# Optimization experiments

Hardware: AMD Instinct MI355X
Metric: run time of the kernel (lower is better)

The kernel has to match this reference:

```python
import jax, jax.numpy as jnp
import numpy as np
from jax import lax

PATCH = 15
WIDTH_DCP = 55


def _box_sum(x, r):
    # AvgPool2d(kernel=2r+1, stride=1, padding=r, count_include_pad=True) * (2r+1)^2;
    # the kernel-size factor cancels in all mean_*/N ratios below.
    return lax.reduce_window(x, 0.0, lax.add, (1, 1, 2 * r + 1, 2 * r + 1),
                             (1, 1, 1, 1), ((0, 0), (0, 0), (r, r), (r, r)))


def _guided_filter(I, p, r, eps):
    Nn = _box_sum(jnp.ones_like(p), r)
    mean_I = _box_sum(I, r) / Nn
    mean_p = _box_sum(p, r) / Nn
    mean_Ip = _box_sum(I * p, r) / Nn
    cov_Ip = mean_Ip - mean_I * mean_p
    mean_II = _box_sum(I * I, r) / Nn
    var_I = mean_II - mean_I * mean_I
    a = cov_Ip / (var_I + eps)
    b = mean_p - a * mean_I
    mean_a = _box_sum(a, r) / Nn
    mean_b = _box_sum(b, r) / Nn
    return mean_a * I + mean_b


def _dark_channel(x):
    d = x.min(axis=1, keepdims=True)
    pad = WIDTH_DCP // 2
    d = jnp.pad(d, ((0, 0), (0, 0), (pad, pad), (pad, pad)), constant_values=1.0)
    return lax.reduce_window(d, jnp.inf, lax.min, (1, 1, WIDTH_DCP, WIDTH_DCP),
                             (1, 1, 1, 1), 'VALID')


def _map_A(x):
    N, C, H, W = x.shape
    dc = _dark_channel(x).reshape(N, -1)
    k = int(H * W * 0.001)
    _, idx = lax.top_k(dc, k)  # brightest dark-channel pixels
    xr = x.reshape(N, 3, -1)
    searched = jnp.take_along_axis(xr, jnp.broadcast_to(idx[:, None, :], (N, 3, k)), axis=2)
    A = searched.mean(axis=2)
    return jnp.broadcast_to(A[:, :, None, None], x.shape)


def _t_bccr(haze, mapA, ps):
    t1 = (mapA - haze) / (mapA - 20.0 / 255.0)
    t2 = (mapA - haze) / (mapA - 300.0 / 255.0)
    t = jnp.maximum(t1, t2).max(axis=1, keepdims=True)
    pad = ps // 2
    t = jnp.pad(t, ((0, 0), (0, 0), (pad, pad), (pad, pad)), constant_values=0.0)
    t = lax.reduce_window(t, -jnp.inf, lax.max, (1, 1, ps, ps), (1, 1, 1, 1), 'VALID')
    return jnp.clip(t, 0.05, 1.0)


def _pad_reshape(data, ps):
    N, C, H, W = data.shape
    pad_H = (ps - H % ps) % ps
    pad_W = (ps - W % ps) % ps
    padded = jnp.pad(data, ((0, 0), (0, 0), (pad_H // 2, pad_H - pad_H // 2),
                            (pad_W // 2, pad_W - pad_W // 2)), mode='edge')
    nH = padded.shape[2] // ps
    nW = padded.shape[3] // ps
    p = padded[:, 0].reshape(N, nH, ps, nW, ps).transpose(0, 1, 3, 2, 4)
    p = p.reshape(N, nH * nW, ps * ps).transpose(0, 2, 1)  # [N, ps*ps, P]
    return p, pad_H // 2, pad_W // 2, nH, nW


def _transmission(S, V1, ps, pixel_number=10, slp_length=0.1):
    X, sH, sW, nH, nW = _pad_reshape(V1, ps)  # [N, pp, P]
    Y, _, _, _, _ = _pad_reshape(S, ps)
    dX = X[:, :, None, :] - X[:, None, :, :]          # [N, pp, pp, P]
    dY = Y[:, :, None, :] - Y[:, None, :, :]
    slope = dY / (dX + 1e-8)
    smask = ((slope > -1) & (slope < 0)).astype(X.dtype)
    scount = smask.sum(axis=2)                         # [N, pp, P]
    pmask = (scount >= 0.5 * ps * ps).astype(X.dtype)
    pcount = pmask.sum(axis=1, keepdims=True)          # [N, 1, P]
    mx = (X * pmask).sum(axis=1, keepdims=True) / (pcount + 1e-5)
    my = (Y * pmask).sum(axis=1, keepdims=True) / (pcount + 1e-5)
    k = ((X * Y * pmask).sum(axis=1, keepdims=True) - pcount * mx * my) / (
        ((X * pmask) ** 2).sum(axis=1, keepdims=True) - pcount * mx ** 2 + 1e-5)
    b = my - k * mx
    t = 1.0 + k / (b + 1e-8)
    length = (1.0 + k ** 2) ** 0.5 * ((X * pmask).max(axis=1, keepdims=True)
                                      - (X + 1e8 * (1.0 - pmask)).min(axis=1, keepdims=True))
    tmask = ((pcount > pixel_number) & (length > slp_length) & (k > -1) & (k < 0)
             & (t > 0.01) & (t < 1 - 0.01)).astype(X.dtype)
    t = (t * tmask).reshape(-1, 1, nH, nW)
    t = jnp.repeat(jnp.repeat(t, ps, axis=2), ps, axis=3)  # nearest upsample x ps
    return t[:, :, sH:S.shape[2] + sH, sW:S.shape[3] + sW]


def _percentile(t, bili=0.05):
    N = t.shape[0]
    flat = jnp.where(t > 0, t, 10.0).reshape(N, -1)
    s = jnp.sort(flat, axis=1)
    n = flat.shape[1]
    idx = min(int(bili * n), n - 1)
    return s[:, idx].reshape(-1, 1, 1, 1)


def _restore(image, ps=PATCH):
    mapA = _map_A(image)
    norm = image / mapA
    mx = norm.max(axis=1, keepdims=True)
    S = 1.0 - norm.min(axis=1, keepdims=True) / (mx + 1e-8)
    V1 = 1.0 / (mx + 1e-8)
    t1 = _transmission(S, V1, ps)
    half = ps // 2
    t2 = _transmission(S[:, :, half:, half:], V1[:, :, half:, half:], ps)
    t2 = jnp.pad(t2, ((0, 0), (0, 0), (half, 0), (half, 0)), constant_values=0.0)
    t_slp = jnp.where((t1 != 0) & (t2 != 0), (t1 + t2) / 2.0,
                      jnp.where(t1 != 0, t1, t2))
    t_bl = _t_bccr(image, mapA, ps)
    t_min = _percentile(t_slp)
    t_fusion = jnp.clip(jnp.where(t_slp > 0, t_slp, t_bl), t_min, 1.0)
    t_ref = _guided_filter(image.mean(axis=1, keepdims=True), t_fusion, 2 * ps, 1e-3)
    return (image - mapA) / t_ref + mapA


def setup_inputs() -> dict:
    key = jax.random.key(0)
    image = jax.random.uniform(key, (1, 3, 480, 480), dtype=jnp.float32)
    return {"image": image}


def reference(image):
    return _restore(image)
```

## Files before the change

kernel.cpp:

```cpp
#include <hip/hip_runtime.h>
#include <math.h>

#define W 480
#define HT 480
#define HW (W*HT)
#define GE (HW/256)
#define PP 225
#define NPATCH 1024
#define EQCAP 8192

struct State {
  unsigned slotP[4];
  unsigned slotK[4];
  float sumA[3];
  unsigned eqCount;
  float A[3];
  unsigned tminbits;
  unsigned eqIdx[EQCAP];
  float tp1[NPATCH];
  float tp2[NPATCH];
};

__device__ __forceinline__ void resolve_level(const unsigned* __restrict__ h,
                                              unsigned k_in, int desc,
                                              unsigned* lds,
                                              unsigned& chosen, unsigned& k_out) {
  int t = threadIdx.x;
  unsigned c = h[desc ? (255 - t) : t];
  lds[t] = c;
  __syncthreads();
  for (int s = 1; s < 256; s <<= 1) {
    unsigned add = (t >= s) ? lds[t - s] : 0u;
    __syncthreads();
    lds[t] += add;
    __syncthreads();
  }
  unsigned incl = lds[t];
  unsigned excl = incl - c;
  if (incl >= k_in && excl < k_in) { lds[256] = (unsigned)t; lds[257] = k_in - excl; }
  __syncthreads();
  unsigned tt = lds[256];
  k_out = lds[257];
  chosen = desc ? (255u - tt) : tt;
  __syncthreads();
}

__global__ __launch_bounds__(512) void k_rowmin(const float* __restrict__ img,
                                                float* __restrict__ rowmin,
                                                State* st, unsigned* __restrict__ hist16) {
  __shared__ float l[534];
  int y = blockIdx.x, t = threadIdx.x;
  int g = y * 512 + t;
  if (g < 65536) hist16[g] = 0u;
  for (int i = t; i < 534; i += 512) {
    int col = i - 27;
    float v = 1.0f;
    if ((unsigned)col < (unsigned)W) {
      int q = y * W + col;
      v = fminf(fminf(img[q], img[HW + q]), img[2 * HW + q]);
    }
    l[i] = v;
  }
  if (g == 0) { st->sumA[0] = 0.f; st->sumA[1] = 0.f; st->sumA[2] = 0.f; st->eqCount = 0u; }
  __syncthreads();
  if (t < W) {
    float m = l[t];
    for (int d = 1; d < 55; ++d) m = fminf(m, l[t + d]);
    rowmin[y * W + t] = m;
  }
}

__global__ __launch_bounds__(256) void k_minV3(const float* __restrict__ rowmin,
                                               float* __restrict__ dc,
                                               unsigned* __restrict__ hist16) {
  __shared__ unsigned short bs[256];
  int t = threadIdx.x;
  int p = blockIdx.x * 256 + t;
  int y = p / W, x = p - y * W;
  int lo = y - 27, hi = y + 27;
  float m = (lo < 0 || hi >= HT) ? 1.0f : INFINITY;
  int lo2 = max(lo, 0), hi2 = min(hi, HT - 1);
  for (int yy = lo2; yy <= hi2; ++yy) m = fminf(m, rowmin[yy * W + x]);
  dc[p] = m;
  unsigned b16 = __float_as_uint(m) >> 16;
  bs[t] = (unsigned short)b16;
  __syncthreads();
  int firstIdx = 256, cnt = 0;
  for (int j = 0; j < 256; ++j) {
    if ((unsigned)bs[j] == b16) { ++cnt; if (j < firstIdx) firstIdx = j; }
  }
  if (firstIdx == t) atomicAdd(&hist16[b16], (unsigned)cnt);
}

__global__ __launch_bounds__(256) void k_resolve16(const unsigned* __restrict__ hist16,
                                                   State* st) {
  __shared__ unsigned lds[258];
  __shared__ unsigned lh[256];
  int t = threadIdx.x;
  const uint4* h4 = (const uint4*)hist16;
  unsigned s = 0;
  for (int i = 0; i < 64; ++i) { uint4 v = h4[t * 64 + i]; s += v.x + v.y + v.z + v.w; }
  lh[t] = s;
  __syncthreads();
  unsigned ct, kc;
  resolve_level(lh, 230u, 1, lds, ct, kc);
  lh[t] = hist16[ct * 256 + t];
  __syncthreads();
  unsigned b, kp;
  resolve_level(lh, kc, 1, lds, b, kp);
  if (t == 0) { st->slotP[0] = (ct << 8) | b; st->slotK[0] = kp; }
}

__global__ __launch_bounds__(256) void k_gather2(const float* __restrict__ dc,
                                                 const float* __restrict__ img, State* st) {
  __shared__ float ls[3];
  __shared__ unsigned lcnt, lbase;
  int t = threadIdx.x;
  if (t == 0) { ls[0] = 0.f; ls[1] = 0.f; ls[2] = 0.f; lcnt = 0u; }
  __syncthreads();
  int p = blockIdx.x * 256 + t;
  unsigned p16 = st->slotP[0];
  unsigned b16 = __float_as_uint(dc[p]) >> 16;
  bool eq = (b16 == p16);
  unsigned my = 0;
  if (b16 > p16) {
    atomicAdd(&ls[0], img[p]);
    atomicAdd(&ls[1], img[HW + p]);
    atomicAdd(&ls[2], img[2 * HW + p]);
  } else if (eq) {
    my = atomicAdd(&lcnt, 1u);
  }
  __syncthreads();
  if (t == 0 && lcnt) lbase = atomicAdd(&st->eqCount, lcnt);
  __syncthreads();
  if (eq) { unsigned pos = lbase + my; if (pos < (unsigned)EQCAP) st->eqIdx[pos] = (unsigned)p; }
  if (t == 0 && (ls[0] != 0.f || ls[1] != 0.f || ls[2] != 0.f)) {
    atomicAdd(&st->sumA[0], ls[0]);
    atomicAdd(&st->sumA[1], ls[1]);
    atomicAdd(&st->sumA[2], ls[2]);
  }
}

__global__ __launch_bounds__(256) void k_finalizeA2(const float* __restrict__ dc,
                                                    const float* __restrict__ img, State* st) {
  __shared__ unsigned lds[258];
  __shared__ unsigned lh[256];
  __shared__ unsigned sIdx[EQCAP];
  __shared__ unsigned short sVal[EQCAP];
  __shared__ float ssum[3];
  int t = threadIdx.x;
  unsigned k = st->slotK[0];
  unsigned ne = st->eqCount; if (ne > (unsigned)EQCAP) ne = EQCAP;
  for (int i = t; i < (int)ne; i += 256) {
    unsigned q = st->eqIdx[i];
    sIdx[i] = q;
    sVal[i] = (unsigned short)(__float_as_uint(dc[q]) & 0xFFFFu);
  }
  if (t < 3) ssum[t] = 0.f;
  __syncthreads();
  unsigned vpfx = 0u;
  for (int lev = 0; lev < 2; ++lev) {
    int s = 8 - 8 * lev;
    lh[t] = 0u;
    __syncthreads();
    for (int i = t; i < (int)ne; i += 256) {
      unsigned v = (unsigned)sVal[i];
      if (lev == 0 || (v >> 8) == (vpfx >> 8))
        atomicAdd(&lh[(v >> s) & 0xFFu], 1u);
    }
    __syncthreads();
    unsigned ch, kn;
    resolve_level(lh, k, 1, lds, ch, kn);
    vpfx |= ch << s;
    k = kn;
  }
  unsigned pfx = 0u;
  for (int lev = 0; lev < 3; ++lev) {
    int s = 16 - 8 * lev;
    lh[t] = 0u;
    __syncthreads();
    for (int i = t; i < (int)ne; i += 256) {
      if ((unsigned)sVal[i] == vpfx) {
        unsigned v = sIdx[i];
        if ((v >> (s + 8)) == (pfx >> (s + 8)))
          atomicAdd(&lh[(v >> s) & 0xFFu], 1u);
      }
    }
    __syncthreads();
    unsigned ch, kn;
    resolve_level(lh, k, 0, lds, ch, kn);
    pfx |= ch << s;
    k = kn;
  }
  float a0 = 0.f, a1 = 0.f, a2 = 0.f;
  for (int i = t; i < (int)ne; i += 256) {
    unsigned v = (unsigned)sVal[i], q = sIdx[i];
    if (v > vpfx || (v == vpfx && q <= pfx)) {
      a0 += img[q]; a1 += img[HW + q]; a2 += img[2 * HW + q];
    }
  }
  atomicAdd(&ssum[0], a0); atomicAdd(&ssum[1], a1); atomicAdd(&ssum[2], a2);
  __syncthreads();
  if (t == 0) {
    st->A[0] = (st->sumA[0] + ssum[0]) / 230.0f;
    st->A[1] = (st->sumA[1] + ssum[1]) / 230.0f;
    st->A[2] = (st->sumA[2] + ssum[2]) / 230.0f;
  }
}

__device__ __forceinline__ float wred_sum(float v) { for (int m = 32; m; m >>= 1) v += __shfl_xor(v, m, 64); return v; }
__device__ __forceinline__ float wred_max(float v) { for (int m = 32; m; m >>= 1) v = fmaxf(v, __shfl_xor(v, m, 64)); return v; }
__device__ __forceinline__ float wred_min(float v) { for (int m = 32; m; m >>= 1) v = fminf(v, __shfl_xor(v, m, 64)); return v; }

__global__ __launch_bounds__(256) void k_mega1(const float* __restrict__ img,
                                               float* __restrict__ mh, State* st) {
  __shared__ float2 XY[PP];
  __shared__ float part[4][8];
  __shared__ float Tl[494];
  int b = blockIdx.x;
  int t = threadIdx.x;
  float A0 = st->A[0], A1 = st->A[1], A2 = st->A[2];
  const float c20 = (float)(20.0 / 255.0);
  const float c300 = (float)(300.0 / 255.0);
  if (b >= 2048) {
    int y = b - 2048;
    for (int i = t; i < 494; i += 256) {
      int col = i - 7;
      float v = 0.0f;
      if ((unsigned)col < (unsigned)W) {
        int q = y * W + col;
        float r = img[q], g = img[HW + q], bl = img[2 * HW + q];
        float t0 = fmaxf((A0 - r) / (A0 - c20), (A0 - r) / (A0 - c300));
        float t1 = fmaxf((A1 - g) / (A1 - c20), (A1 - g) / (A1 - c300));
        float t2 = fmaxf((A2 - bl) / (A2 - c20), (A2 - bl) / (A2 - c300));
        v = fmaxf(fmaxf(t0, t1), t2);
      }
      Tl[i] = v;
    }
    __syncthreads();
    for (int x = t; x < W; x += 256) {
      float m = -INFINITY;
      for (int d = 0; d < 15; ++d) m = fmaxf(m, Tl[x + d]);
      mh[y * W + x] = m;
    }
    return;
  }
  int mode = b >> 10;
  int pid = b & 1023;
  int ph = pid >> 5, pw = pid & 31;
  if (t < PP) {
    int r = t / 15, c = t - (t / 15) * 15;
    int y, x;
    if (mode == 0) { y = ph * 15 + r; x = pw * 15 + c; }
    else {
      y = ph * 15 + r + 4; y = (y < 7) ? 7 : ((y > 479) ? 479 : y);
      x = pw * 15 + c + 4; x = (x < 7) ? 7 : ((x > 479) ? 479 : x);
    }
    int q = y * W + x;
    float rr = img[q], gg = img[HW + q], bb = img[2 * HW + q];
    float nr = rr / A0, ng = gg / A1, nb = bb / A2;
    float mx = fmaxf(fmaxf(nr, ng), nb);
    float mn = fminf(fminf(nr, ng), nb);
    float d = mx + 1e-8f;
    XY[t] = make_float2(1.0f / d, 1.0f - mn / d);
  }
  __syncthreads();
  float xi = 0.f, yi = 0.f;
  int cnt = 0;
  if (t < PP) {
    xi = XY[t].x; yi = XY[t].y;
    #pragma unroll 5
    for (int j = 0; j < PP; ++j) {
      float2 o = XY[j];
      float dY = yi - o.y;
      float D = (xi - o.x) + 1e-8f;
      cnt += ((dY * D < 0.0f) && (fabsf(dY) < fabsf(D))) ? 1 : 0;
    }
  }
  float pmf = (t < PP && cnt >= 113) ? 1.0f : 0.0f;
  float xm = xi * pmf, ym = yi * pmf;
  float v0 = wred_sum(pmf);
  float v1 = wred_sum(xm);
  float v2 = wred_sum(ym);
  float v3 = wred_sum(xm * ym);
  float v4 = wred_sum(xm * xm);
  float v5 = wred_max((t < PP) ? xm : -INFINITY);
  float v6 = wred_min((t < PP) ? (xi + 1e8f * (1.0f - pmf)) : INFINITY);
  int wid = t >> 6, lane = t & 63;
  if (lane == 0) {
    part[wid][0] = v0; part[wid][1] = v1; part[wid][2] = v2; part[wid][3] = v3;
    part[wid][4] = v4; part[wid][5] = v5; part[wid][6] = v6;
  }
  __syncthreads();
  if (t == 0) {
    float pcount = 0.f, sx = 0.f, sy = 0.f, sxy = 0.f, sxx = 0.f;
    float mxX = -INFINITY, mnX = INFINITY;
    for (int w2 = 0; w2 < 4; ++w2) {
      pcount += part[w2][0]; sx += part[w2][1]; sy += part[w2][2];
      sxy += part[w2][3]; sxx += part[w2][4];
      mxX = fmaxf(mxX, part[w2][5]); mnX = fminf(mnX, part[w2][6]);
    }
    float den = pcount + 1e-5f;
    float mxv = sx / den, myv = sy / den;
    float kk = (sxy - pcount * mxv * myv) / (sxx - pcount * (mxv * mxv) + 1e-5f);
    float bb = myv - kk * mxv;
    float tt = 1.0f + kk / (bb + 1e-8f);
    float len = sqrtf(1.0f + kk * kk) * (mxX - mnX);
    bool m = (pcount > 10.0f) && (len > 0.1f) && (kk > -1.0f) && (kk < 0.0f)
             && (tt > 0.01f) && (tt < 0.99f);
    float res = tt * (m ? 1.0f : 0.0f);
    if (mode == 0) st->tp1[pid] = res; else st->tp2[pid] = res;
  }
}

__global__ __launch_bounds__(256) void k_maxV_pct(const float* __restrict__ mh,
                                                  float* __restrict__ tb, State* st) {
  __shared__ unsigned lh[256];
  __shared__ unsigned lds[258];
  __shared__ float tp1s[NPATCH], tp2s[NPATCH];
  int b = blockIdx.x;
  int t = threadIdx.x;
  if (b < GE) {
    int p = b * 256 + t;
    int y = p / W, x = p - y * W;
    float m = -INFINITY;
    for (int d = -7; d <= 7; ++d) {
      int yy = y + d;
      float v = ((unsigned)yy < (unsigned)HT) ? mh[yy * W + x] : 0.0f;
      m = fmaxf(m, v);
    }
    tb[p] = fminf(fmaxf(m, 0.05f), 1.0f);
    return;
  }
  for (int i = t; i < NPATCH; i += 256) { tp1s[i] = st->tp1[i]; tp2s[i] = st->tp2[i]; }
  __syncthreads();
  unsigned prefix = 0u, k = 11521u;
  for (int level = 0; level < 4; ++level) {
    lh[t] = 0u;
    __syncthreads();
    unsigned mask = (level == 0) ? 0u : (0xFFFFFFFFu << (32 - 8 * level));
    int shift = 24 - 8 * level;
    for (int i = t; i < NPATCH; i += 256) {
      int ph = i >> 5, pw = i & 31;
      float a = tp1s[i];
      int rcnt[2], ridx[2], ccnt[2], cidx[2];
      if (ph == 0) { rcnt[0] = 7; ridx[0] = -1; rcnt[1] = 8; ridx[1] = 0; }
      else         { rcnt[0] = 4; ridx[0] = ph - 1; rcnt[1] = 11; ridx[1] = ph; }
      if (pw == 0) { ccnt[0] = 7; cidx[0] = -1; ccnt[1] = 8; cidx[1] = 0; }
      else         { ccnt[0] = 4; cidx[0] = pw - 1; ccnt[1] = 11; cidx[1] = pw; }
      for (int ri = 0; ri < 2; ++ri)
        for (int ci = 0; ci < 2; ++ci) {
          unsigned area = (unsigned)(rcnt[ri] * ccnt[ci]);
          float bb = 0.0f;
          if (ridx[ri] >= 0 && cidx[ci] >= 0) bb = tp2s[ridx[ri] * 32 + cidx[ci]];
          float r;
          if (a != 0.0f && bb != 0.0f) r = (a + bb) / 2.0f;
          else r = (a != 0.0f) ? a : bb;
          float u = (r > 0.0f) ? r : 10.0f;
          unsigned bits = __float_as_uint(u);
          if ((bits & mask) == prefix)
            atomicAdd(&lh[(bits >> shift) & 0xFFu], area);
        }
    }
    __syncthreads();
    unsigned ch, kn;
    resolve_level(lh, k, 0, lds, ch, kn);
    prefix |= ch << shift;
    k = kn;
  }
  if (t == 0) st->tminbits = prefix;
}

__global__ __launch_bounds__(512) void k_gf1h(const float* __restrict__ img,
                                              const float* __restrict__ tb,
                                              const State* __restrict__ st,
                                              float4* __restrict__ box4) {
  __shared__ float tp1s[NPATCH], tp2s[NPATCH];
  __shared__ float Pl[540], Il[540];
  int y = blockIdx.x, t = threadIdx.x;
  for (int i = t; i < NPATCH; i += 512) { tp1s[i] = st->tp1[i]; tp2s[i] = st->tp2[i]; }
  __syncthreads();
  float tmin = __uint_as_float(st->tminbits);
  int c1row = (y / 15) * 32;
  bool c2ok = (y >= 7);
  int c2row = c2ok ? ((y - 4) / 15) * 32 : 0;
  for (int i = t; i < 540; i += 512) {
    int col = i - 30;
    float pv = 0.0f, iv = 0.0f;
    if ((unsigned)col < (unsigned)W) {
      int q = y * W + col;
      float a = tp1s[c1row + col / 15];
      float bb = 0.0f;
      if (c2ok && col >= 7) bb = tp2s[c2row + (col - 4) / 15];
      float r;
      if (a != 0.0f && bb != 0.0f) r = (a + bb) / 2.0f;
      else r = (a != 0.0f) ? a : bb;
      float v = (r > 0.0f) ? r : tb[q];
      v = (v < tmin) ? tmin : v;
      v = (v > 1.0f) ? 1.0f : v;
      pv = v;
      iv = ((img[q] + img[HW + q]) + img[2 * HW + q]) / 3.0f;
    }
    Pl[i] = pv; Il[i] = iv;
  }
  __syncthreads();
  if (t < W) {
    float sI = 0.f, sP = 0.f, sIp = 0.f, sII = 0.f;
    for (int d = 0; d < 61; ++d) {
      float iv = Il[t + d], pv = Pl[t + d];
      sI += iv; sP += pv; sIp += iv * pv; sII += iv * iv;
    }
    box4[y * W + t] = make_float4(sI, sP, sIp, sII);
  }
}

__global__ __launch_bounds__(512) void k_gf1vh(const float4* __restrict__ box4,
                                               float2* __restrict__ hab) {
  __shared__ float2 l[540];
  int y = blockIdx.x, t = threadIdx.x;
  float2 v = make_float2(0.f, 0.f);
  if (t < W) {
    float sI = 0.f, sP = 0.f, sIp = 0.f, sII = 0.f;
    for (int d = -30; d <= 30; ++d) {
      int yy = y + d;
      if ((unsigned)yy < (unsigned)HT) {
        float4 b = box4[yy * W + t];
        sI += b.x; sP += b.y; sIp += b.z; sII += b.w;
      }
    }
    int ny = min(y + 30, HT - 1) - max(y - 30, 0) + 1;
    int nx = min(t + 30, W - 1) - max(t - 30, 0) + 1;
    float Nn = (float)(ny * nx);
    float mI = sI / Nn, mP = sP / Nn, mIp = sIp / Nn, mII = sII / Nn;
    float cov = mIp - mI * mP;
    float var = mII - mI * mI;
    float av = cov / (var + 1e-3f);
    v = make_float2(av, mP - av * mI);
  }
  if (t < 30) { l[t] = make_float2(0.f, 0.f); l[510 + t] = make_float2(0.f, 0.f); }
  if (t < W) l[30 + t] = v;
  __syncthreads();
  if (t < W) {
    float sa = 0.f, sb = 0.f;
    for (int d = 0; d < 61; ++d) { float2 u = l[t + d]; sa += u.x; sb += u.y; }
    hab[y * W + t] = make_float2(sa, sb);
  }
}

__global__ __launch_bounds__(256) void k_gf2vfin(const float2* __restrict__ hab,
                                                 const float* __restrict__ img,
                                                 const State* __restrict__ st,
                                                 float* __restrict__ out) {
  int p = blockIdx.x * 256 + threadIdx.x;
  int y = p / W, x = p - y * W;
  float sa = 0.f, sb = 0.f;
  for (int d = -30; d <= 30; ++d) {
    int yy = y + d;
    if ((unsigned)yy < (unsigned)HT) { float2 v = hab[yy * W + x]; sa += v.x; sb += v.y; }
  }
  int ny = min(y + 30, HT - 1) - max(y - 30, 0) + 1;
  int nx = min(x + 30, W - 1) - max(x - 30, 0) + 1;
  float Nn = (float)(ny * nx);
  float r = img[p], g = img[HW + p], bl = img[2 * HW + p];
  float Iv = ((r + g) + bl) / 3.0f;
  float tref = (sa / Nn) * Iv + (sb / Nn);
  float A0 = st->A[0], A1 = st->A[1], A2 = st->A[2];
  out[p]          = (r  - A0) / tref + A0;
  out[HW + p]     = (g  - A1) / tref + A1;
  out[2 * HW + p] = (bl - A2) / tref + A2;
}

extern "C" void kernel_launch(void* const* d_in, const int* in_sizes, int n_in,
                              void* d_out, int out_size, void* d_ws, size_t ws_size,
                              hipStream_t stream) {
  (void)in_sizes; (void)n_in; (void)out_size; (void)ws_size;
  const float* img = (const float*)d_in[0];
  float* out = (float*)d_out;
  State* st = (State*)d_ws;
  unsigned* hist16 = (unsigned*)((char*)d_ws + 65536);
  float* sb = (float*)((char*)d_ws + 65536 + 262144);
  float* bufA = sb;
  float* bufB = sb + HW;
  float4* box4 = (float4*)(sb + 2 * HW);
  float2* hab  = (float2*)(sb + 6 * HW);

  dim3 b256(256), b512(512);
  dim3 ge(GE), rows(HT);

  k_rowmin<<<rows, b512, 0, stream>>>(img, bufB, st, hist16);
  k_minV3<<<ge, b256, 0, stream>>>(bufB, bufA, hist16);
  k_resolve16<<<dim3(1), b256, 0, stream>>>(hist16, st);
  k_gather2<<<ge, b256, 0, stream>>>(bufA, img, st);
  k_finalizeA2<<<dim3(1), b256, 0, stream>>>(bufA, img, st);
  k_mega1<<<dim3(2048 + HT), b256, 0, stream>>>(img, bufB, st);
  k_maxV_pct<<<dim3(GE + 1), b256, 0, stream>>>(bufB, bufA, st);
  k_gf1h<<<rows, b512, 0, stream>>>(img, bufA, st, box4);
  k_gf1vh<<<rows, b512, 0, stream>>>(box4, hab);
  k_gf2vfin<<<ge, b256, 0, stream>>>(hab, img, st, out);
}
```

Before: 185.5 us.

## Fuse all pipeline stages into one cooperative persistent kernel with grid syncs

Replaces the ten separate kernel launches with a single cooperative kernel of 512 persistent blocks that loops over rows and tiles for each stage and separates stages with grid-wide syncs. Serial single-block stages run on block 0 while the other blocks wait at the next grid sync. This targets per-launch overhead and inter-kernel gaps. The cost is that 512-thread row kernels now run as 256-thread blocks striding over rows, so parallelism per stage is capped at the grid size, and each grid sync adds its own latency.

```diff
diff --git a/kernel.cpp b/kernel.cpp
--- a/kernel.cpp
+++ b/kernel.cpp
@@ -1,13 +1,17 @@
 #include <hip/hip_runtime.h>
+#include <hip/hip_cooperative_groups.h>
 #include <math.h>
 
 #define W 480
 #define HT 480
 #define HW (W*HT)
-#define GE (HW/256)
+#define NT (HW/256)
 #define PP 225
 #define NPATCH 1024
 #define EQCAP 8192
+#define GRID 512
+
+namespace cg = cooperative_groups;
 
 struct State {
   unsigned slotP[4];
@@ -45,429 +49,442 @@
   __syncthreads();
 }
 
-__global__ __launch_bounds__(512) void k_rowmin(const float* __restrict__ img,
-                                                float* __restrict__ rowmin,
-                                                State* st, unsigned* __restrict__ hist16) {
-  __shared__ float l[534];
-  int y = blockIdx.x, t = threadIdx.x;
-  int g = y * 512 + t;
-  if (g < 65536) hist16[g] = 0u;
-  for (int i = t; i < 534; i += 512) {
-    int col = i - 27;
-    float v = 1.0f;
-    if ((unsigned)col < (unsigned)W) {
-      int q = y * W + col;
-      v = fminf(fminf(img[q], img[HW + q]), img[2 * HW + q]);
-    }
-    l[i] = v;
-  }
-  if (g == 0) { st->sumA[0] = 0.f; st->sumA[1] = 0.f; st->sumA[2] = 0.f; st->eqCount = 0u; }
-  __syncthreads();
-  if (t < W) {
-    float m = l[t];
-    for (int d = 1; d < 55; ++d) m = fminf(m, l[t + d]);
-    rowmin[y * W + t] = m;
-  }
-}
-
-__global__ __launch_bounds__(256) void k_minV3(const float* __restrict__ rowmin,
-                                               float* __restrict__ dc,
-                                               unsigned* __restrict__ hist16) {
-  __shared__ unsigned short bs[256];
-  int t = threadIdx.x;
-  int p = blockIdx.x * 256 + t;
-  int y = p / W, x = p - y * W;
-  int lo = y - 27, hi = y + 27;
-  float m = (lo < 0 || hi >= HT) ? 1.0f : INFINITY;
-  int lo2 = max(lo, 0), hi2 = min(hi, HT - 1);
-  for (int yy = lo2; yy <= hi2; ++yy) m = fminf(m, rowmin[yy * W + x]);
-  dc[p] = m;
-  unsigned b16 = __float_as_uint(m) >> 16;
-  bs[t] = (unsigned short)b16;
-  __syncthreads();
-  int firstIdx = 256, cnt = 0;
-  for (int j = 0; j < 256; ++j) {
-    if ((unsigned)bs[j] == b16) { ++cnt; if (j < firstIdx) firstIdx = j; }
-  }
-  if (firstIdx == t) atomicAdd(&hist16[b16], (unsigned)cnt);
-}
-
-__global__ __launch_bounds__(256) void k_resolve16(const unsigned* __restrict__ hist16,
-                                                   State* st) {
-  __shared__ unsigned lds[258];
-  __shared__ unsigned lh[256];
-  int t = threadIdx.x;
-  const uint4* h4 = (const uint4*)hist16;
-  unsigned s = 0;
-  for (int i = 0; i < 64; ++i) { uint4 v = h4[t * 64 + i]; s += v.x + v.y + v.z + v.w; }
-  lh[t] = s;
-  __syncthreads();
-  unsigned ct, kc;
-  resolve_level(lh, 230u, 1, lds, ct, kc);
-  lh[t] = hist16[ct * 256 + t];
-  __syncthreads();
-  unsigned b, kp;
-  resolve_level(lh, kc, 1, lds, b, kp);
-  if (t == 0) { st->slotP[0] = (ct << 8) | b; st->slotK[0] = kp; }
-}
-
-__global__ __launch_bounds__(256) void k_gather2(const float* __restrict__ dc,
-                                                 const float* __restrict__ img, State* st) {
-  __shared__ float ls[3];
-  __shared__ unsigned lcnt, lbase;
-  int t = threadIdx.x;
-  if (t == 0) { ls[0] = 0.f; ls[1] = 0.f; ls[2] = 0.f; lcnt = 0u; }
-  __syncthreads();
-  int p = blockIdx.x * 256 + t;
-  unsigned p16 = st->slotP[0];
-  unsigned b16 = __float_as_uint(dc[p]) >> 16;
-  bool eq = (b16 == p16);
-  unsigned my = 0;
-  if (b16 > p16) {
-    atomicAdd(&ls[0], img[p]);
-    atomicAdd(&ls[1], img[HW + p]);
-    atomicAdd(&ls[2], img[2 * HW + p]);
-  } else if (eq) {
-    my = atomicAdd(&lcnt, 1u);
-  }
-  __syncthreads();
-  if (t == 0 && lcnt) lbase = atomicAdd(&st->eqCount, lcnt);
-  __syncthreads();
-  if (eq) { unsigned pos = lbase + my; if (pos < (unsigned)EQCAP) st->eqIdx[pos] = (unsigned)p; }
-  if (t == 0 && (ls[0] != 0.f || ls[1] != 0.f || ls[2] != 0.f)) {
-    atomicAdd(&st->sumA[0], ls[0]);
-    atomicAdd(&st->sumA[1], ls[1]);
-    atomicAdd(&st->sumA[2], ls[2]);
-  }
-}
-
-__global__ __launch_bounds__(256) void k_finalizeA2(const float* __restrict__ dc,
-                                                    const float* __restrict__ img, State* st) {
-  __shared__ unsigned lds[258];
-  __shared__ unsigned lh[256];
-  __shared__ unsigned sIdx[EQCAP];
-  __shared__ unsigned short sVal[EQCAP];
-  __shared__ float ssum[3];
-  int t = threadIdx.x;
-  unsigned k = st->slotK[0];
-  unsigned ne = st->eqCount; if (ne > (unsigned)EQCAP) ne = EQCAP;
-  for (int i = t; i < (int)ne; i += 256) {
-    unsigned q = st->eqIdx[i];
-    sIdx[i] = q;
-    sVal[i] = (unsigned short)(__float_as_uint(dc[q]) & 0xFFFFu);
-  }
-  if (t < 3) ssum[t] = 0.f;
-  __syncthreads();
-  unsigned vpfx = 0u;
-  for (int lev = 0; lev < 2; ++lev) {
-    int s = 8 - 8 * lev;
-    lh[t] = 0u;
-    __syncthreads();
-    for (int i = t; i < (int)ne; i += 256) {
-      unsigned v = (unsigned)sVal[i];
-      if (lev == 0 || (v >> 8) == (vpfx >> 8))
-        atomicAdd(&lh[(v >> s) & 0xFFu], 1u);
-    }
-    __syncthreads();
-    unsigned ch, kn;
-    resolve_level(lh, k, 1, lds, ch, kn);
-    vpfx |= ch << s;
-    k = kn;
-  }
-  unsigned pfx = 0u;
-  for (int lev = 0; lev < 3; ++lev) {
-    int s = 16 - 8 * lev;
-    lh[t] = 0u;
-    __syncthreads();
-    for (int i = t; i < (int)ne; i += 256) {
-      if ((unsigned)sVal[i] == vpfx) {
-        unsigned v = sIdx[i];
-        if ((v >> (s + 8)) == (pfx >> (s + 8)))
-          atomicAdd(&lh[(v >> s) & 0xFFu], 1u);
-      }
-    }
-    __syncthreads();
-    unsigned ch, kn;
-    resolve_level(lh, k, 0, lds, ch, kn);
-    pfx |= ch << s;
-    k = kn;
-  }
-  float a0 = 0.f, a1 = 0.f, a2 = 0.f;
-  for (int i = t; i < (int)ne; i += 256) {
-    unsigned v = (unsigned)sVal[i], q = sIdx[i];
-    if (v > vpfx || (v == vpfx && q <= pfx)) {
-      a0 += img[q]; a1 += img[HW + q]; a2 += img[2 * HW + q];
-    }
-  }
-  atomicAdd(&ssum[0], a0); atomicAdd(&ssum[1], a1); atomicAdd(&ssum[2], a2);
-  __syncthreads();
-  if (t == 0) {
-    st->A[0] = (st->sumA[0] + ssum[0]) / 230.0f;
-    st->A[1] = (st->sumA[1] + ssum[1]) / 230.0f;
-    st->A[2] = (st->sumA[2] + ssum[2]) / 230.0f;
-  }
-}
-
 __device__ __forceinline__ float wred_sum(float v) { for (int m = 32; m; m >>= 1) v += __shfl_xor(v, m, 64); return v; }
 __device__ __forceinline__ float wred_max(float v) { for (int m = 32; m; m >>= 1) v = fmaxf(v, __shfl_xor(v, m, 64)); return v; }
 __device__ __forceinline__ float wred_min(float v) { for (int m = 32; m; m >>= 1) v = fminf(v, __shfl_xor(v, m, 64)); return v; }
 
-__global__ __launch_bounds__(256) void k_mega1(const float* __restrict__ img,
-                                               float* __restrict__ mh, State* st) {
-  __shared__ float2 XY[PP];
-  __shared__ float part[4][8];
-  __shared__ float Tl[494];
-  int b = blockIdx.x;
-  int t = threadIdx.x;
-  float A0 = st->A[0], A1 = st->A[1], A2 = st->A[2];
-  const float c20 = (float)(20.0 / 255.0);
-  const float c300 = (float)(300.0 / 255.0);
-  if (b >= 2048) {
-    int y = b - 2048;
-    for (int i = t; i < 494; i += 256) {
-      int col = i - 7;
-      float v = 0.0f;
-      if ((unsigned)col < (unsigned)W) {
-        int q = y * W + col;
-        float r = img[q], g = img[HW + q], bl = img[2 * HW + q];
-        float t0 = fmaxf((A0 - r) / (A0 - c20), (A0 - r) / (A0 - c300));
-        float t1 = fmaxf((A1 - g) / (A1 - c20), (A1 - g) / (A1 - c300));
-        float t2 = fmaxf((A2 - bl) / (A2 - c20), (A2 - bl) / (A2 - c300));
-        v = fmaxf(fmaxf(t0, t1), t2);
-      }
-      Tl[i] = v;
-    }
+__global__ __launch_bounds__(256, 2) void k_all(const float* __restrict__ img,
+                                                float* __restrict__ out,
+                                                State* __restrict__ st,
+                                                unsigned* __restrict__ hist16,
+                                                float* __restrict__ bufA,
+                                                float* __restrict__ bufB,
+                                                float4* __restrict__ box4,
+                                                float2* __restrict__ hab) {
+  __shared__ __align__(16) char smem[51264];
+  unsigned* s_lds = (unsigned*)smem;
+  unsigned* s_lh  = (unsigned*)(smem + 1040);
+  char* ph = smem + 2080;
+  cg::grid_group grid = cg::this_grid();
+  const int t = threadIdx.x;
+  const int bid = blockIdx.x;
+  const int nb = gridDim.x;
+
+  {
+    int g = bid * 256 + t;
+    if (g < 65536) hist16[g] = 0u;
+    if (g == 0) { st->sumA[0] = 0.f; st->sumA[1] = 0.f; st->sumA[2] = 0.f; st->eqCount = 0u; }
+  }
+  {
+    float* l = (float*)ph;
+    for (int y = bid; y < HT; y += nb) {
+      for (int i = t; i < 534; i += 256) {
+        int col = i - 27;
+        float v = 1.0f;
+        if ((unsigned)col < (unsigned)W) {
+          int q = y * W + col;
+          v = fminf(fminf(img[q], img[HW + q]), img[2 * HW + q]);
+        }
+        l[i] = v;
+      }
+      __syncthreads();
+      for (int x = t; x < W; x += 256) {
+        float m = l[x];
+        for (int d = 1; d < 55; ++d) m = fminf(m, l[x + d]);
+        bufB[y * W + x] = m;
+      }
+      __syncthreads();
+    }
+  }
+  grid.sync();
+  {
+    unsigned short* bs = (unsigned short*)ph;
+    for (int vb = bid; vb < NT; vb += nb) {
+      int p = vb * 256 + t;
+      int y = p / W, x = p - y * W;
+      int lo = y - 27, hi = y + 27;
+      float m = (lo < 0 || hi >= HT) ? 1.0f : INFINITY;
+      int lo2 = max(lo, 0), hi2 = min(hi, HT - 1);
+      for (int yy = lo2; yy <= hi2; ++yy) m = fminf(m, bufB[yy * W + x]);
+      bufA[p] = m;
+      unsigned b16 = __float_as_uint(m) >> 16;
+      bs[t] = (unsigned short)b16;
+      __syncthreads();
+      int firstIdx = 256, cnt = 0;
+      for (int j = 0; j < 256; ++j) {
+        if ((unsigned)bs[j] == b16) { ++cnt; if (j < firstIdx) firstIdx = j; }
+      }
+      if (firstIdx == t) atomicAdd(&hist16[b16], (unsigned)cnt);
+      __syncthreads();
+    }
+  }
+  grid.sync();
+  if (bid == 0) {
+    const uint4* h4 = (const uint4*)hist16;
+    unsigned s = 0;
+    for (int i = 0; i < 64; ++i) { uint4 v = h4[t * 64 + i]; s += v.x + v.y + v.z + v.w; }
+    s_lh[t] = s;
     __syncthreads();
-    for (int x = t; x < W; x += 256) {
-      float m = -INFINITY;
-      for (int d = 0; d < 15; ++d) m = fmaxf(m, Tl[x + d]);
-      mh[y * W + x] = m;
-    }
-    return;
-  }
-  int mode = b >> 10;
-  int pid = b & 1023;
-  int ph = pid >> 5, pw = pid & 31;
-  if (t < PP) {
-    int r = t / 15, c = t - (t / 15) * 15;
-    int y, x;
-    if (mode == 0) { y = ph * 15 + r; x = pw * 15 + c; }
-    else {
-      y = ph * 15 + r + 4; y = (y < 7) ? 7 : ((y > 479) ? 479 : y);
-      x = pw * 15 + c + 4; x = (x < 7) ? 7 : ((x > 479) ? 479 : x);
-    }
-    int q = y * W + x;
-    float rr = img[q], gg = img[HW + q], bb = img[2 * HW + q];
-    float nr = rr / A0, ng = gg / A1, nb = bb / A2;
-    float mx = fmaxf(fmaxf(nr, ng), nb);
-    float mn = fminf(fminf(nr, ng), nb);
-    float d = mx + 1e-8f;
-    XY[t] = make_float2(1.0f / d, 1.0f - mn / d);
-  }
-  __syncthreads();
-  float xi = 0.f, yi = 0.f;
-  int cnt = 0;
-  if (t < PP) {
-    xi = XY[t].x; yi = XY[t].y;
-    #pragma unroll 5
-    for (int j = 0; j < PP; ++j) {
-      float2 o = XY[j];
-      float dY = yi - o.y;
-      float D = (xi - o.x) + 1e-8f;
-      cnt += ((dY * D < 0.0f) && (fabsf(dY) < fabsf(D))) ? 1 : 0;
-    }
-  }
-  float pmf = (t < PP && cnt >= 113) ? 1.0f : 0.0f;
-  float xm = xi * pmf, ym = yi * pmf;
-  float v0 = wred_sum(pmf);
-  float v1 = wred_sum(xm);
-  float v2 = wred_sum(ym);
-  float v3 = wred_sum(xm * ym);
-  float v4 = wred_sum(xm * xm);
-  float v5 = wred_max((t < PP) ? xm : -INFINITY);
-  float v6 = wred_min((t < PP) ? (xi + 1e8f * (1.0f - pmf)) : INFINITY);
-  int wid = t >> 6, lane = t & 63;
-  if (lane == 0) {
-    part[wid][0] = v0; part[wid][1] = v1; part[wid][2] = v2; part[wid][3] = v3;
-    part[wid][4] = v4; part[wid][5] = v5; part[wid][6] = v6;
-  }
-  __syncthreads();
-  if (t == 0) {
-    float pcount = 0.f, sx = 0.f, sy = 0.f, sxy = 0.f, sxx = 0.f;
-    float mxX = -INFINITY, mnX = INFINITY;
-    for (int w2 = 0; w2 < 4; ++w2) {
-      pcount += part[w2][0]; sx += part[w2][1]; sy += part[w2][2];
-      sxy += part[w2][3]; sxx += part[w2][4];
-      mxX = fmaxf(mxX, part[w2][5]); mnX = fminf(mnX, part[w2][6]);
-    }
-    float den = pcount + 1e-5f;
-    float mxv = sx / den, myv = sy / den;
-    float kk = (sxy - pcount * mxv * myv) / (sxx - pcount * (mxv * mxv) + 1e-5f);
-    float bb = myv - kk * mxv;
-    float tt = 1.0f + kk / (bb + 1e-8f);
-    float len = sqrtf(1.0f + kk * kk) * (mxX - mnX);
-    bool m = (pcount > 10.0f) && (len > 0.1f) && (kk > -1.0f) && (kk < 0.0f)
-             && (tt > 0.01f) && (tt < 0.99f);
-    float res = tt * (m ? 1.0f : 0.0f);
-    if (mode == 0) st->tp1[pid] = res; else st->tp2[pid] = res;
-  }
-}
-
-__global__ __launch_bounds__(256) void k_maxV_pct(const float* __restrict__ mh,
-                                                  float* __restrict__ tb, State* st) {
-  __shared__ unsigned lh[256];
-  __shared__ unsigned lds[258];
-  __shared__ float tp1s[NPATCH], tp2s[NPATCH];
-  int b = blockIdx.x;
-  int t = threadIdx.x;
-  if (b < GE) {
-    int p = b * 256 + t;
-    int y = p / W, x = p - y * W;
-    float m = -INFINITY;
-    for (int d = -7; d <= 7; ++d) {
-      int yy = y + d;
-      float v = ((unsigned)yy < (unsigned)HT) ? mh[yy * W + x] : 0.0f;
-      m = fmaxf(m, v);
-    }
-    tb[p] = fminf(fmaxf(m, 0.05f), 1.0f);
-    return;
-  }
-  for (int i = t; i < NPATCH; i += 256) { tp1s[i] = st->tp1[i]; tp2s[i] = st->tp2[i]; }
-  __syncthreads();
-  unsigned prefix = 0u, k = 11521u;
-  for (int level = 0; level < 4; ++level) {
-    lh[t] = 0u;
+    unsigned ct, kc;
+    resolve_level(s_lh, 230u, 1, s_lds, ct, kc);
+    s_lh[t] = hist16[ct * 256 + t];
     __syncthreads();
-    unsigned mask = (level == 0) ? 0u : (0xFFFFFFFFu << (32 - 8 * level));
-    int shift = 24 - 8 * level;
-    for (int i = t; i < NPATCH; i += 256) {
-      int ph = i >> 5, pw = i & 31;
-      float a = tp1s[i];
-      int rcnt[2], ridx[2], ccnt[2], cidx[2];
-      if (ph == 0) { rcnt[0] = 7; ridx[0] = -1; rcnt[1] = 8; ridx[1] = 0; }
-      else         { rcnt[0] = 4; ridx[0] = ph - 1; rcnt[1] = 11; ridx[1] = ph; }
-      if (pw == 0) { ccnt[0] = 7; cidx[0] = -1; ccnt[1] = 8; cidx[1] = 0; }
-      else         { ccnt[0] = 4; cidx[0] = pw - 1; ccnt[1] = 11; cidx[1] = pw; }
-      for (int ri = 0; ri < 2; ++ri)
-        for (int ci = 0; ci < 2; ++ci) {
-          unsigned area = (unsigned)(rcnt[ri] * ccnt[ci]);
+    unsigned b, kp;
+    resolve_level(s_lh, kc, 1, s_lds, b, kp);
+    if (t == 0) { st->slotP[0] = (ct << 8) | b; st->slotK[0] = kp; }
+  }
+  grid.sync();
+  {
+    float* ls = (float*)ph;
+    unsigned* lu = (unsigned*)(ph + 16);
+    unsigned p16 = st->slotP[0];
+    for (int vb = bid; vb < NT; vb += nb) {
+      if (t == 0) { ls[0] = 0.f; ls[1] = 0.f; ls[2] = 0.f; lu[0] = 0u; }
+      __syncthreads();
+      int p = vb * 256 + t;
+      unsigned b16 = __float_as_uint(bufA[p]) >> 16;
+      bool eq = (b16 == p16);
+      unsigned my = 0;
+      if (b16 > p16) {
+        atomicAdd(&ls[0], img[p]);
+        atomicAdd(&ls[1], img[HW + p]);
+        atomicAdd(&ls[2], img[2 * HW + p]);
+      } else if (eq) {
+        my = atomicAdd(&lu[0], 1u);
+      }
+      __syncthreads();
+      if (t == 0 && lu[0]) lu[1] = atomicAdd(&st->eqCount, lu[0]);
+      __syncthreads();
+      if (eq) { unsigned pos = lu[1] + my; if (pos < (unsigned)EQCAP) st->eqIdx[pos] = (unsigned)p; }
+      if (t == 0 && (ls[0] != 0.f || ls[1] != 0.f || ls[2] != 0.f)) {
+        atomicAdd(&st->sumA[0], ls[0]);
+        atomicAdd(&st->sumA[1], ls[1]);
+        atomicAdd(&st->sumA[2], ls[2]);
+      }
+      __syncthreads();
+    }
+  }
+  grid.sync();
+  if (bid == 0) {
+    float* ssum = (float*)ph;
+    unsigned short* sVal = (unsigned short*)(ph + 16);
+    unsigned* sIdx = (unsigned*)(ph + 16 + 2 * EQCAP);
+    unsigned k = st->slotK[0];
+    unsigned ne = st->eqCount; if (ne > (unsigned)EQCAP) ne = EQCAP;
+    for (int i = t; i < (int)ne; i += 256) {
+      unsigned q = st->eqIdx[i];
+      sIdx[i] = q;
+      sVal[i] = (unsigned short)(__float_as_uint(bufA[q]) & 0xFFFFu);
+    }
+    if (t < 3) ssum[t] = 0.f;
+    __syncthreads();
+    unsigned vpfx = 0u;
+    for (int lev = 0; lev < 2; ++lev) {
+      int s = 8 - 8 * lev;
+      s_lh[t] = 0u;
+      __syncthreads();
+      for (int i = t; i < (int)ne; i += 256) {
+        unsigned v = (unsigned)sVal[i];
+        if (lev == 0 || (v >> 8) == (vpfx >> 8))
+          atomicAdd(&s_lh[(v >> s) & 0xFFu], 1u);
+      }
+      __syncthreads();
+      unsigned ch, kn;
+      resolve_level(s_lh, k, 1, s_lds, ch, kn);
+      vpfx |= ch << s;
+      k = kn;
+    }
+    unsigned pfx = 0u;
+    for (int lev = 0; lev < 3; ++lev) {
+      int s = 16 - 8 * lev;
+      s_lh[t] = 0u;
+      __syncthreads();
+      for (int i = t; i < (int)ne; i += 256) {
+        if ((unsigned)sVal[i] == vpfx) {
+          unsigned v = sIdx[i];
+          if ((v >> (s + 8)) == (pfx >> (s + 8)))
+            atomicAdd(&s_lh[(v >> s) & 0xFFu], 1u);
+        }
+      }
+      __syncthreads();
+      unsigned ch, kn;
+      resolve_level(s_lh, k, 0, s_lds, ch, kn);
+      pfx |= ch << s;
+      k = kn;
+    }
+    float a0 = 0.f, a1 = 0.f, a2 = 0.f;
+    for (int i = t; i < (int)ne; i += 256) {
+      unsigned v = (unsigned)sVal[i], q = sIdx[i];
+      if (v > vpfx || (v == vpfx && q <= pfx)) {
+        a0 += img[q]; a1 += img[HW + q]; a2 += img[2 * HW + q];
+      }
+    }
+    atomicAdd(&ssum[0], a0); atomicAdd(&ssum[1], a1); atomicAdd(&ssum[2], a2);
+    __syncthreads();
+    if (t == 0) {
+      st->A[0] = (st->sumA[0] + ssum[0]) / 230.0f;
+      st->A[1] = (st->sumA[1] + ssum[1]) / 230.0f;
+      st->A[2] = (st->sumA[2] + ssum[2]) / 230.0f;
+    }
+  }
+  grid.sync();
+  {
+    float A0 = st->A[0], A1 = st->A[1], A2 = st->A[2];
+    const float c20 = (float)(20.0 / 255.0);
+    const float c300 = (float)(300.0 / 255.0);
+    float2* XY = (float2*)ph;
+    float* part = (float*)(ph + 1808);
+    float* Tl = (float*)(ph + 1952);
+    for (int vb = bid; vb < 2048 + HT; vb += nb) {
+      if (vb >= 2048) {
+        int y = vb - 2048;
+        for (int i = t; i < 494; i += 256) {
+          int col = i - 7;
+          float v = 0.0f;
+          if ((unsigned)col < (unsigned)W) {
+            int q = y * W + col;
+            float r = img[q], g = img[HW + q], bl = img[2 * HW + q];
+            float t0 = fmaxf((A0 - r) / (A0 - c20), (A0 - r) / (A0 - c300));
+            float t1 = fmaxf((A1 - g) / (A1 - c20), (A1 - g) / (A1 - c300));
+            float t2 = fmaxf((A2 - bl) / (A2 - c20), (A2 - bl) / (A2 - c300));
+            v = fmaxf(fmaxf(t0, t1), t2);
+          }
+          Tl[i] = v;
+        }
+        __syncthreads();
+        for (int x = t; x < W; x += 256) {
+          float m = -INFINITY;
+          for (int d = 0; d < 15; ++d) m = fmaxf(m, Tl[x + d]);
+          bufB[y * W + x] = m;
+        }
+        __syncthreads();
+      } else {
+        int mode = vb >> 10;
+        int pid = vb & 1023;
+        int phh = pid >> 5, pw = pid & 31;
+        if (t < PP) {
+          int r = t / 15, c = t - (t / 15) * 15;
+          int y, x;
+          if (mode == 0) { y = phh * 15 + r; x = pw * 15 + c; }
+          else {
+            y = phh * 15 + r + 4; y = (y < 7) ? 7 : ((y > 479) ? 479 : y);
+            x = pw * 15 + c + 4; x = (x < 7) ? 7 : ((x > 479) ? 479 : x);
+          }
+          int q = y * W + x;
+          float rr = img[q], gg = img[HW + q], bb = img[2 * HW + q];
+          float nr = rr / A0, ng = gg / A1, nbv = bb / A2;
+          float mx = fmaxf(fmaxf(nr, ng), nbv);
+          float mn = fminf(fminf(nr, ng), nbv);
+          float d = mx + 1e-8f;
+          XY[t] = make_float2(1.0f / d, 1.0f - mn / d);
+        }
+        __syncthreads();
+        float xi = 0.f, yi = 0.f;
+        int cnt = 0;
+        if (t < PP) {
+          xi = XY[t].x; yi = XY[t].y;
+          #pragma unroll 5
+          for (int j = 0; j < PP; ++j) {
+            float2 o = XY[j];
+            float dY = yi - o.y;
+            float D = (xi - o.x) + 1e-8f;
+            cnt += ((dY * D < 0.0f) && (fabsf(dY) < fabsf(D))) ? 1 : 0;
+          }
+        }
+        float pmf = (t < PP && cnt >= 113) ? 1.0f : 0.0f;
+        float xm = xi * pmf, ym = yi * pmf;
+        float v0 = wred_sum(pmf);
+        float v1 = wred_sum(xm);
+        float v2 = wred_sum(ym);
+        float v3 = wred_sum(xm * ym);
+        float v4 = wred_sum(xm * xm);
+        float v5 = wred_max((t < PP) ? xm : -INFINITY);
+        float v6 = wred_min((t < PP) ? (xi + 1e8f * (1.0f - pmf)) : INFINITY);
+        int wid = t >> 6, lane = t & 63;
+        if (lane == 0) {
+          part[wid * 8 + 0] = v0; part[wid * 8 + 1] = v1; part[wid * 8 + 2] = v2;
+          part[wid * 8 + 3] = v3; part[wid * 8 + 4] = v4; part[wid * 8 + 5] = v5;
+          part[wid * 8 + 6] = v6;
+        }
+        __syncthreads();
+        if (t == 0) {
+          float pcount = 0.f, sx = 0.f, sy = 0.f, sxy = 0.f, sxx = 0.f;
+          float mxX = -INFINITY, mnX = INFINITY;
+          for (int w2 = 0; w2 < 4; ++w2) {
+            pcount += part[w2 * 8 + 0]; sx += part[w2 * 8 + 1]; sy += part[w2 * 8 + 2];
+            sxy += part[w2 * 8 + 3]; sxx += part[w2 * 8 + 4];
+            mxX = fmaxf(mxX, part[w2 * 8 + 5]); mnX = fminf(mnX, part[w2 * 8 + 6]);
+          }
+          float den = pcount + 1e-5f;
+          float mxv = sx / den, myv = sy / den;
+          float kk = (sxy - pcount * mxv * myv) / (sxx - pcount * (mxv * mxv) + 1e-5f);
+          float bb2 = myv - kk * mxv;
+          float tt = 1.0f + kk / (bb2 + 1e-8f);
+          float len = sqrtf(1.0f + kk * kk) * (mxX - mnX);
+          bool m = (pcount > 10.0f) && (len > 0.1f) && (kk > -1.0f) && (kk < 0.0f)
+                   && (tt > 0.01f) && (tt < 0.99f);
+          float res = tt * (m ? 1.0f : 0.0f);
+          if (mode == 0) st->tp1[pid] = res; else st->tp2[pid] = res;
+        }
+        __syncthreads();
+      }
+    }
+  }
+  grid.sync();
+  {
+    float* tp1s = (float*)ph;
+    float* tp2s = (float*)(ph + 4096);
+    for (int vb = bid; vb < NT + 1; vb += nb) {
+      if (vb < NT) {
+        int p = vb * 256 + t;
+        int y = p / W, x = p - y * W;
+        float m = -INFINITY;
+        for (int d = -7; d <= 7; ++d) {
+          int yy = y + d;
+          float v = ((unsigned)yy < (unsigned)HT) ? bufB[yy * W + x] : 0.0f;
+          m = fmaxf(m, v);
+        }
+        bufA[p] = fminf(fmaxf(m, 0.05f), 1.0f);
+      } else {
+        for (int i = t; i < NPATCH; i += 256) { tp1s[i] = st->tp1[i]; tp2s[i] = st->tp2[i]; }
+        __syncthreads();
+        unsigned prefix = 0u, k = 11521u;
+        for (int level = 0; level < 4; ++level) {
+          s_lh[t] = 0u;
+          __syncthreads();
+          unsigned mask = (level == 0) ? 0u : (0xFFFFFFFFu << (32 - 8 * level));
+          int shift = 24 - 8 * level;
+          for (int i = t; i < NPATCH; i += 256) {
+            int phh = i >> 5, pw = i & 31;
+            float a = tp1s[i];
+            int rcnt[2], ridx[2], ccnt[2], cidx[2];
+            if (phh == 0) { rcnt[0] = 7; ridx[0] = -1; rcnt[1] = 8; ridx[1] = 0; }
+            else          { rcnt[0] = 4; ridx[0] = phh - 1; rcnt[1] = 11; ridx[1] = phh; }
+            if (pw == 0) { ccnt[0] = 7; cidx[0] = -1; ccnt[1] = 8; cidx[1] = 0; }
+            else         { ccnt[0] = 4; cidx[0] = pw - 1; ccnt[1] = 11; cidx[1] = pw; }
+            for (int ri = 0; ri < 2; ++ri)
+              for (int ci = 0; ci < 2; ++ci) {
+                unsigned area = (unsigned)(rcnt[ri] * ccnt[ci]);
+                float bb = 0.0f;
+                if (ridx[ri] >= 0 && cidx[ci] >= 0) bb = tp2s[ridx[ri] * 32 + cidx[ci]];
+                float r;
+                if (a != 0.0f && bb != 0.0f) r = (a + bb) / 2.0f;
+                else r = (a != 0.0f) ? a : bb;
+                float u = (r > 0.0f) ? r : 10.0f;
+                unsigned bits = __float_as_uint(u);
+                if ((bits & mask) == prefix)
+                  atomicAdd(&s_lh[(bits >> shift) & 0xFFu], area);
+              }
+          }
+          __syncthreads();
+          unsigned ch, kn;
+          resolve_level(s_lh, k, 0, s_lds, ch, kn);
+          prefix |= ch << shift;
+          k = kn;
+        }
+        if (t == 0) st->tminbits = prefix;
+        __syncthreads();
+      }
+    }
+  }
+  grid.sync();
+  {
+    float* tp1s = (float*)ph;
+    float* tp2s = (float*)(ph + 4096);
+    float* Pl = (float*)(ph + 8192);
+    float* Il = (float*)(ph + 10352);
+    for (int y = bid; y < HT; y += nb) {
+      for (int i = t; i < NPATCH; i += 256) { tp1s[i] = st->tp1[i]; tp2s[i] = st->tp2[i]; }
+      __syncthreads();
+      float tmin = __uint_as_float(st->tminbits);
+      int c1row = (y / 15) * 32;
+      bool c2ok = (y >= 7);
+      int c2row = c2ok ? ((y - 4) / 15) * 32 : 0;
+      for (int i = t; i < 540; i += 256) {
+        int col = i - 30;
+        float pv = 0.0f, iv = 0.0f;
+        if ((unsigned)col < (unsigned)W) {
+          int q = y * W + col;
+          float a = tp1s[c1row + col / 15];
           float bb = 0.0f;
-          if (ridx[ri] >= 0 && cidx[ci] >= 0) bb = tp2s[ridx[ri] * 32 + cidx[ci]];
+          if (c2ok && col >= 7) bb = tp2s[c2row + (col - 4) / 15];
           float r;
           if (a != 0.0f && bb != 0.0f) r = (a + bb) / 2.0f;
           else r = (a != 0.0f) ? a : bb;
-          float u = (r > 0.0f) ? r : 10.0f;
-          unsigned bits = __float_as_uint(u);
-          if ((bits & mask) == prefix)
-            atomicAdd(&lh[(bits >> shift) & 0xFFu], area);
-        }
-    }
-    __syncthreads();
-    unsigned ch, kn;
-    resolve_level(lh, k, 0, lds, ch, kn);
-    prefix |= ch << shift;
-    k = kn;
-  }
-  if (t == 0) st->tminbits = prefix;
-}
-
-__global__ __launch_bounds__(512) void k_gf1h(const float* __restrict__ img,
-                                              const float* __restrict__ tb,
-                                              const State* __restrict__ st,
-                                              float4* __restrict__ box4) {
-  __shared__ float tp1s[NPATCH], tp2s[NPATCH];
-  __shared__ float Pl[540], Il[540];
-  int y = blockIdx.x, t = threadIdx.x;
-  for (int i = t; i < NPATCH; i += 512) { tp1s[i] = st->tp1[i]; tp2s[i] = st->tp2[i]; }
-  __syncthreads();
-  float tmin = __uint_as_float(st->tminbits);
-  int c1row = (y / 15) * 32;
-  bool c2ok = (y >= 7);
-  int c2row = c2ok ? ((y - 4) / 15) * 32 : 0;
-  for (int i = t; i < 540; i += 512) {
-    int col = i - 30;
-    float pv = 0.0f, iv = 0.0f;
-    if ((unsigned)col < (unsigned)W) {
-      int q = y * W + col;
-      float a = tp1s[c1row + col / 15];
-      float bb = 0.0f;
-      if (c2ok && col >= 7) bb = tp2s[c2row + (col - 4) / 15];
-      float r;
-      if (a != 0.0f && bb != 0.0f) r = (a + bb) / 2.0f;
-      else r = (a != 0.0f) ? a : bb;
-      float v = (r > 0.0f) ? r : tb[q];
-      v = (v < tmin) ? tmin : v;
-      v = (v > 1.0f) ? 1.0f : v;
-      pv = v;
-      iv = ((img[q] + img[HW + q]) + img[2 * HW + q]) / 3.0f;
-    }
-    Pl[i] = pv; Il[i] = iv;
-  }
-  __syncthreads();
-  if (t < W) {
-    float sI = 0.f, sP = 0.f, sIp = 0.f, sII = 0.f;
-    for (int d = 0; d < 61; ++d) {
-      float iv = Il[t + d], pv = Pl[t + d];
-      sI += iv; sP += pv; sIp += iv * pv; sII += iv * iv;
-    }
-    box4[y * W + t] = make_float4(sI, sP, sIp, sII);
-  }
-}
-
-__global__ __launch_bounds__(512) void k_gf1vh(const float4* __restrict__ box4,
-                                               float2* __restrict__ hab) {
-  __shared__ float2 l[540];
-  int y = blockIdx.x, t = threadIdx.x;
-  float2 v = make_float2(0.f, 0.f);
-  if (t < W) {
-    float sI = 0.f, sP = 0.f, sIp = 0.f, sII = 0.f;
-    for (int d = -30; d <= 30; ++d) {
-      int yy = y + d;
-      if ((unsigned)yy < (unsigned)HT) {
-        float4 b = box4[yy * W + t];
-        sI += b.x; sP += b.y; sIp += b.z; sII += b.w;
-      }
-    }
-    int ny = min(y + 30, HT - 1) - max(y - 30, 0) + 1;
-    int nx = min(t + 30, W - 1) - max(t - 30, 0) + 1;
-    float Nn = (float)(ny * nx);
-    float mI = sI / Nn, mP = sP / Nn, mIp = sIp / Nn, mII = sII / Nn;
-    float cov = mIp - mI * mP;
-    float var = mII - mI * mI;
-    float av = cov / (var + 1e-3f);
-    v = make_float2(av, mP - av * mI);
-  }
-  if (t < 30) { l[t] = make_float2(0.f, 0.f); l[510 + t] = make_float2(0.f, 0.f); }
-  if (t < W) l[30 + t] = v;
-  __syncthreads();
-  if (t < W) {
-    float sa = 0.f, sb = 0.f;
-    for (int d = 0; d < 61; ++d) { float2 u = l[t + d]; sa += u.x; sb += u.y; }
-    hab[y * W + t] = make_float2(sa, sb);
-  }
-}
-
-__global__ __launch_bounds__(256) void k_gf2vfin(const float2* __restrict__ hab,
-                                                 const float* __restrict__ img,
-                                                 const State* __restrict__ st,
-                                                 float* __restrict__ out) {
-  int p = blockIdx.x * 256 + threadIdx.x;
-  int y = p / W, x = p - y * W;
-  float sa = 0.f, sb = 0.f;
-  for (int d = -30; d <= 30; ++d) {
-    int yy = y + d;
-    if ((unsigned)yy < (unsigned)HT) { float2 v = hab[yy * W + x]; sa += v.x; sb += v.y; }
-  }
-  int ny = min(y + 30, HT - 1) - max(y - 30, 0) + 1;
-  int nx = min(x + 30, W - 1) - max(x - 30, 0) + 1;
-  float Nn = (float)(ny * nx);
-  float r = img[p], g = img[HW + p], bl = img[2 * HW + p];
-  float Iv = ((r + g) + bl) / 3.0f;
-  float tref = (sa / Nn) * Iv + (sb / Nn);
-  float A0 = st->A[0], A1 = st->A[1], A2 = st->A[2];
-  out[p]          = (r  - A0) / tref + A0;
-  out[HW + p]     = (g  - A1) / tref + A1;
-  out[2 * HW + p] = (bl - A2) / tref + A2;
+          float v = (r > 0.0f) ? r : bufA[q];
+          v = (v < tmin) ? tmin : v;
+          v = (v > 1.0f) ? 1.0f : v;
+          pv = v;
+          iv = ((img[q] + img[HW + q]) + img[2 * HW + q]) / 3.0f;
+        }
+        Pl[i] = pv; Il[i] = iv;
+      }
+      __syncthreads();
+      for (int x = t; x < W; x += 256) {
+        float sI = 0.f, sP = 0.f, sIp = 0.f, sII = 0.f;
+        for (int d = 0; d < 61; ++d) {
+          float iv = Il[x + d], pv = Pl[x + d];
+          sI += iv; sP += pv; sIp += iv * pv; sII += iv * iv;
+        }
+        box4[y * W + x] = make_float4(sI, sP, sIp, sII);
+      }
+      __syncthreads();
+    }
+  }
+  grid.sync();
+  {
+    float2* l = (float2*)ph;
+    for (int y = bid; y < HT; y += nb) {
+      if (t < 30) { l[t] = make_float2(0.f, 0.f); l[510 + t] = make_float2(0.f, 0.f); }
+      for (int x = t; x < W; x += 256) {
+        float sI = 0.f, sP = 0.f, sIp = 0.f, sII = 0.f;
+        for (int d = -30; d <= 30; ++d) {
+          int yy = y + d;
+          if ((unsigned)yy < (unsigned)HT) {
+            float4 b = box4[yy * W + x];
+            sI += b.x; sP += b.y; sIp += b.z; sII += b.w;
+          }
+        }
+        int ny = min(y + 30, HT - 1) - max(y - 30, 0) + 1;
+        int nx = min(x + 30, W - 1) - max(x - 30, 0) + 1;
+        float Nn = (float)(ny * nx);
+        float mI = sI / Nn, mP = sP / Nn, mIp = sIp / Nn, mII = sII / Nn;
+        float cov = mIp - mI * mP;
+        float var = mII - mI * mI;
+        float av = cov / (var + 1e-3f);
+        l[30 + x] = make_float2(av, mP - av * mI);
+      }
+      __syncthreads();
+      for (int x = t; x < W; x += 256) {
+        float sa = 0.f, sb = 0.f;
+        for (int d = 0; d < 61; ++d) { float2 u = l[x + d]; sa += u.x; sb += u.y; }
+        hab[y * W + x] = make_float2(sa, sb);
+      }
+      __syncthreads();
+    }
+  }
+  grid.sync();
+  {
+    for (int vb = bid; vb < NT; vb += nb) {
+      int p = vb * 256 + t;
+      int y = p / W, x = p - y * W;
+      float sa = 0.f, sb = 0.f;
+      for (int d = -30; d <= 30; ++d) {
+        int yy = y + d;
+        if ((unsigned)yy < (unsigned)HT) { float2 v = hab[yy * W + x]; sa += v.x; sb += v.y; }
+      }
+      int ny = min(y + 30, HT - 1) - max(y - 30, 0) + 1;
+      int nx = min(x + 30, W - 1) - max(x - 30, 0) + 1;
+      float Nn = (float)(ny * nx);
+      float r = img[p], g = img[HW + p], bl = img[2 * HW + p];
+      float Iv = ((r + g) + bl) / 3.0f;
+      float tref = (sa / Nn) * Iv + (sb / Nn);
+      float A0 = st->A[0], A1 = st->A[1], A2 = st->A[2];
+      out[p]          = (r  - A0) / tref + A0;
+      out[HW + p]     = (g  - A1) / tref + A1;
+      out[2 * HW + p] = (bl - A2) / tref + A2;
+    }
+  }
 }
 
 extern "C" void kernel_launch(void* const* d_in, const int* in_sizes, int n_in,
@@ -484,17 +501,7 @@
   float4* box4 = (float4*)(sb + 2 * HW);
   float2* hab  = (float2*)(sb + 6 * HW);
 
-  dim3 b256(256), b512(512);
-  dim3 ge(GE), rows(HT);
-
-  k_rowmin<<<rows, b512, 0, stream>>>(img, bufB, st, hist16);
-  k_minV3<<<ge, b256, 0, stream>>>(bufB, bufA, hist16);
-  k_resolve16<<<dim3(1), b256, 0, stream>>>(hist16, st);
-  k_gather2<<<ge, b256, 0, stream>>>(bufA, img, st);
-  k_finalizeA2<<<dim3(1), b256, 0, stream>>>(bufA, img, st);
-  k_mega1<<<dim3(2048 + HT), b256, 0, stream>>>(img, bufB, st);
-  k_maxV_pct<<<dim3(GE + 1), b256, 0, stream>>>(bufB, bufA, st);
-  k_gf1h<<<rows, b512, 0, stream>>>(img, bufA, st, box4);
-  k_gf1vh<<<rows, b512, 0, stream>>>(box4, hab);
-  k_gf2vfin<<<ge, b256, 0, stream>>>(hab, img, st, out);
+  void* args[] = { (void*)&img, (void*)&out, (void*)&st, (void*)&hist16,
+                   (void*)&bufA, (void*)&bufB, (void*)&box4, (void*)&hab };
+  hipLaunchCooperativeKernel((const void*)k_all, dim3(GRID), dim3(256), args, 0, stream);
 }
```

After: 693.9 us. +274.0%, slower.
